# Performance work log

Measured on AMD Instinct MI355X. Metric: run time of the kernel, lower is better.

Reference implementation:

```python
import jax, jax.numpy as jnp
import numpy as np

B, N, K = 8, 4096, 16          # batch, points, kNN neighbors
IN_F, D, L, NUM_CLS = 3, 128, 2, 40  # in_features, hidden dim, transformer blocks, classes


def setup_inputs() -> dict:
    key = jax.random.key(0)
    ks = jax.random.split(key, 13)

    def w(k, shape):
        fan_in = shape[-2]
        return (jax.random.normal(k, shape, jnp.float32) / np.sqrt(fan_in).astype(np.float32))

    return {
        "features": jax.random.normal(ks[0], (B, N, IN_F), jnp.float32),
        "pos": jax.random.normal(ks[1], (B, N, 3), jnp.float32),
        "W_embed": w(ks[2], (IN_F, D)),
        "Wq": w(ks[3], (L, D, D)),
        "Wk": w(ks[4], (L, D, D)),
        "Wv": w(ks[5], (L, D, D)),
        "P1": w(ks[6], (L, 3, D)),   # position-encoding MLP layer 1
        "P2": w(ks[7], (L, D, D)),   # position-encoding MLP layer 2
        "G1": w(ks[8], (L, D, D)),   # attention (gamma) MLP layer 1
        "G2": w(ks[9], (L, D, D)),   # attention (gamma) MLP layer 2
        "Wo": w(ks[10], (L, D, D)),  # output projection per block
        "W_cls1": w(ks[11], (D, D)),
        "W_cls2": w(ks[12], (D, NUM_CLS)),
    }


def _gather(x, idx):
    # x: [B,N,C], idx: [B,N,K] -> [B,N,K,C]
    return jax.vmap(lambda xb, ib: xb[ib])(x, idx)


def _forward(features, pos, W_embed, Wq, Wk, Wv, P1, P2, G1, G2, Wo, W_cls1, W_cls2):
    # point-wise embedding MLP
    x = jax.nn.relu(features @ W_embed)  # [B,N,D]

    # kNN in euclidean space (indices, incl. self)
    sq = jnp.sum(pos * pos, axis=-1)                      # [B,N]
    d2 = sq[:, :, None] + sq[:, None, :] - 2.0 * jnp.einsum("bnc,bmc->bnm", pos, pos)
    _, idx = jax.lax.top_k(-d2, K)                        # [B,N,K]

    rel = pos[:, :, None, :] - _gather(pos, idx)          # [B,N,K,3]

    for l in range(L):
        q = x @ Wq[l]                                     # [B,N,D]
        k = x @ Wk[l]
        v = x @ Wv[l]
        kj = _gather(k, idx)                              # [B,N,K,D]
        vj = _gather(v, idx)
        # relative position encoding MLP
        delta = jax.nn.relu(rel @ P1[l]) @ P2[l]          # [B,N,K,D]
        # vector attention: gamma MLP over (q_i - k_j + delta)
        g = q[:, :, None, :] - kj + delta
        logits = jax.nn.relu(g @ G1[l]) @ G2[l]           # [B,N,K,D]
        attn = jax.nn.softmax(logits, axis=2)             # over K neighbors
        agg = jnp.sum(attn * (vj + delta), axis=2)        # [B,N,D]
        x = x + agg @ Wo[l]                               # residual

    pooled = jnp.max(x, axis=1)                           # [B,D] global max pool
    h = jax.nn.relu(pooled @ W_cls1)
    return h @ W_cls2                                     # [B,NUM_CLS]


def reference(features, pos, W_embed, Wq, Wk, Wv, P1, P2, G1, G2, Wo, W_cls1, W_cls2):
    return _forward(features, pos, W_embed, Wq, Wk, Wv, P1, P2, G1, G2, Wo, W_cls1, W_cls2)
```

## Files before the change

kernel.cpp:

```cpp
#include <hip/hip_runtime.h>
#include <float.h>

#define BB 8
#define NN 4096
#define KNN 16
#define Dh 128
#define NPTS (BB*NN)
#define NPART 8
#define PARTSZ (NN/NPART)

typedef __attribute__((ext_vector_type(8))) short bf16x8;
typedef __attribute__((ext_vector_type(8))) unsigned short u16x8;
typedef __attribute__((ext_vector_type(4))) float f32x4;

#define MFMA16(a,b,c) __builtin_amdgcn_mfma_f32_16x16x32_bf16(a,b,c,0,0,0)

__device__ __forceinline__ unsigned short f2b(float f) {
  union { float f; unsigned u; } v; v.f = f;
  unsigned r = v.u + 0x7fff + ((v.u >> 16) & 1);
  return (unsigned short)(r >> 16);
}
__device__ __forceinline__ float b2f(unsigned short s) {
  union { unsigned u; float f; } v; v.u = ((unsigned)s) << 16; return v.f;
}

__global__ __launch_bounds__(256) void embed_kernel(
    const float* __restrict__ f, const float* __restrict__ We, float* __restrict__ x) {
  int i = blockIdx.x * 256 + threadIdx.x;
  if (i >= NPTS * Dh) return;
  int p = i >> 7, d = i & 127;
  float f0 = f[p*3+0], f1 = f[p*3+1], f2 = f[p*3+2];
  float v = f0 * We[0*Dh + d] + f1 * We[1*Dh + d] + f2 * We[2*Dh + d];
  x[i] = fmaxf(v, 0.f);
}

__global__ __launch_bounds__(256) void knn_part_kernel(
    const float* __restrict__ pos, unsigned short* __restrict__ pidx) {
  __shared__ float4 cand[PARTSZ];
  int b = blockIdx.z, part = blockIdx.y;
  const float* pb = pos + (size_t)b * NN * 3;
  int c0 = part * PARTSZ;
  for (int i = threadIdx.x; i < PARTSZ; i += 256) {
    float X = pb[(c0+i)*3+0], Y = pb[(c0+i)*3+1], Z = pb[(c0+i)*3+2];
    cand[i] = make_float4(X, Y, Z, X*X + Y*Y + Z*Z);
  }
  __syncthreads();

  int q = blockIdx.x * 256 + threadIdx.x;
  float qx = pb[q*3+0], qy = pb[q*3+1], qz = pb[q*3+2];
  float qs = qx*qx + qy*qy + qz*qz;

  float val[KNN]; int ind[KNN];
  float cmax; int cslot;

  #pragma unroll
  for (int t = 0; t < KNN; t++) {
    float4 c = cand[t];
    val[t] = qs + c.w - 2.f*(qx*c.x + qy*c.y + qz*c.z);
    ind[t] = t;
  }
  cmax = val[0]; cslot = 0;
  #pragma unroll
  for (int i = 1; i < KNN; i++)
    if (val[i] >= cmax) { cmax = val[i]; cslot = i; }

  float bv0 = 0.f, bv1 = 0.f, bv2 = 0.f, bv3 = 0.f;
  int   bi0 = 0,   bi1 = 0,   bi2 = 0,   bi3 = 0;
  int   cnt = 0;

#define DRAIN_SLOT(S, BV, BI)                                      \
  { bool act = ((S) < cnt) && ((BV) < cmax);                       \
    if (__ballot(act)) {                                           \
      _Pragma("unroll")                                            \
      for (int i = 0; i < KNN; i++) {                              \
        bool r = act && (i == cslot);                              \
        val[i] = r ? (BV) : val[i];                                \
        ind[i] = r ? (BI) : ind[i];                                \
      }                                                            \
      cmax = val[0]; cslot = 0;                                    \
      _Pragma("unroll")                                            \
      for (int i = 1; i < KNN; i++)                                \
        if (val[i] >= cmax) { cmax = val[i]; cslot = i; }          \
    } }
#define DRAIN_ALL                                                  \
  { DRAIN_SLOT(0, bv0, bi0) DRAIN_SLOT(1, bv1, bi1)                \
    DRAIN_SLOT(2, bv2, bi2) DRAIN_SLOT(3, bv3, bi3) cnt = 0; }

  for (int m = KNN; m < PARTSZ; m++) {
    float4 c = cand[m];
    float d2 = qs + c.w - 2.f*(qx*c.x + qy*c.y + qz*c.z);
    if (d2 < cmax) {
      bv0 = (cnt == 0) ? d2 : bv0;  bi0 = (cnt == 0) ? m : bi0;
      bv1 = (cnt == 1) ? d2 : bv1;  bi1 = (cnt == 1) ? m : bi1;
      bv2 = (cnt == 2) ? d2 : bv2;  bi2 = (cnt == 2) ? m : bi2;
      bv3 = (cnt == 3) ? d2 : bv3;  bi3 = (cnt == 3) ? m : bi3;
      cnt++;
    }
    if (__ballot(cnt == 4)) DRAIN_ALL
  }
  if (__ballot(cnt > 0)) DRAIN_ALL

#undef DRAIN_SLOT
#undef DRAIN_ALL

  size_t base = ((size_t)(b*NN + q) * NPART + part) * KNN;
  #pragma unroll
  for (int i = 0; i < KNN; i++) pidx[base + i] = (unsigned short)(b*NN + c0 + ind[i]);
}

__global__ __launch_bounds__(256) void knn_merge_kernel(
    const float* __restrict__ pos, const unsigned short* __restrict__ pidx,
    unsigned short* __restrict__ idxout) {
  int p = blockIdx.x * 256 + threadIdx.x;
  float qx = pos[p*3+0], qy = pos[p*3+1], qz = pos[p*3+2];
  float qs = qx*qx + qy*qy + qz*qz;

  float val[KNN]; int ind[KNN];
  #pragma unroll
  for (int i = 0; i < KNN; i++) { val[i] = FLT_MAX; ind[i] = 0; }
  float cmax = FLT_MAX; int cslot = 0;

  for (int t = 0; t < NPART*KNN; t++) {
    int j = pidx[(size_t)p*NPART*KNN + t];
    float X = pos[j*3+0], Y = pos[j*3+1], Z = pos[j*3+2];
    float sq = X*X + Y*Y + Z*Z;
    float d2 = qs + sq - 2.f*(qx*X + qy*Y + qz*Z);
    if (d2 < cmax) {
      #pragma unroll
      for (int i = 0; i < KNN; i++) if (i == cslot) { val[i] = d2; ind[i] = j; }
      cmax = val[0]; cslot = 0;
      #pragma unroll
      for (int i = 1; i < KNN; i++) if (val[i] >= cmax) { cmax = val[i]; cslot = i; }
    }
  }
  #pragma unroll
  for (int i = 0; i < KNN; i++) idxout[(size_t)p*KNN + i] = (unsigned short)ind[i];
}

__global__ __launch_bounds__(256) void wprep_all_kernel(
    const float* __restrict__ W0, const float* __restrict__ W1,
    const float* __restrict__ W2, const float* __restrict__ W3,
    const float* __restrict__ W4, const float* __restrict__ W5,
    const float* __restrict__ W6, unsigned short* __restrict__ wT) {
  const float* srcs[7] = {W0, W1, W2, W3, W4, W5, W6};
  int z = blockIdx.z, m = blockIdx.y;
  const float* W = srcs[z] + m*16384;
  unsigned short* WT = wT + z*32768 + m*16384;
  int t = blockIdx.x * 256 + threadIdx.x;
  int o = t >> 7, i = t & 127;
  WT[o*128 + i] = f2b(W[i*128 + o]);
}

__global__ __launch_bounds__(256) void qkv_kernel(
    const float* __restrict__ x,
    const unsigned short* __restrict__ QT, const unsigned short* __restrict__ KT,
    const unsigned short* __restrict__ VT,
    unsigned short* __restrict__ qb, unsigned short* __restrict__ kb,
    unsigned short* __restrict__ vb) {
  int w = threadIdx.x >> 6, l = threadIdx.x & 63;
  int lr = l & 15, lg = l >> 4;
  int R = blockIdx.x * 64 + w * 16;
  const float* xr = x + (size_t)(R + lr) * Dh + lg * 8;
  bf16x8 a[4];
  #pragma unroll
  for (int kt = 0; kt < 4; kt++) {
    bf16x8 av;
    #pragma unroll
    for (int j = 0; j < 8; j++) av[j] = (short)f2b(xr[kt*32 + j]);
    a[kt] = av;
  }
  const unsigned short* Ws[3] = {QT, KT, VT};
  unsigned short* Os[3] = {qb, kb, vb};
  #pragma unroll
  for (int m = 0; m < 3; m++) {
    const unsigned short* W = Ws[m];
    unsigned short* O = Os[m];
    #pragma unroll
    for (int n = 0; n < 8; n++) {
      f32x4 c = {0.f, 0.f, 0.f, 0.f};
      #pragma unroll
      for (int kt = 0; kt < 4; kt++)
        c = MFMA16(a[kt], *(const bf16x8*)&W[(n*16 + lr)*Dh + kt*32 + lg*8], c);
      #pragma unroll
      for (int r = 0; r < 4; r++)
        O[(size_t)(R + lg*4 + r)*Dh + n*16 + lr] = f2b(c[r]);
    }
  }
}

__global__ __launch_bounds__(512, 2) void fused_mega_kernel(
    const unsigned short* __restrict__ qb, const unsigned short* __restrict__ kb,
    const unsigned short* __restrict__ vb,
    const unsigned short* __restrict__ idxb, const float* __restrict__ pos,
    const float* __restrict__ P1,
    const unsigned short* __restrict__ P2T, const unsigned short* __restrict__ G1T,
    const unsigned short* __restrict__ G2T, unsigned short* __restrict__ aggb) {
  __shared__ __align__(16) unsigned short wB[3][16384];
  __shared__ __align__(16) unsigned short trans[8][2048];
  int tid = threadIdx.x;
  int wv = tid >> 6, l = tid & 63;
  int lr = l & 15, lg = l >> 4;
  const int swz = (lr & 7) << 3;

  {
    const unsigned short* srcs[3] = {P2T, G1T, G2T};
    #pragma unroll
    for (int z = 0; z < 3; z++) {
      const unsigned short* src = srcs[z];
      for (int t = tid * 8; t < 16384; t += 512 * 8) {
        int dst = t ^ (((t >> 7) & 7) << 3);
        *(u16x8*)&wB[z][dst] = *(const u16x8*)&src[t];
      }
    }
  }
  __syncthreads();

  unsigned short* tb = trans[wv];
  int p0 = blockIdx.x * 128 + wv * 16;

  #pragma unroll 1
  for (int i = 0; i < 16; i++) {
    int p = p0 + i;

    int jA = idxb[(size_t)p*KNN + lr];
    int jC[4];
    #pragma unroll
    for (int r = 0; r < 4; r++) jC[r] = idxb[(size_t)p*KNN + lg*4 + r];

    float px0 = pos[p*3+0], py0 = pos[p*3+1], pz0 = pos[p*3+2];
    float rx = px0 - pos[jA*3+0], ry = py0 - pos[jA*3+1], rz = pz0 - pos[jA*3+2];

    bf16x8 aT[4];
    #pragma unroll
    for (int kt = 0; kt < 4; kt++) {
      bf16x8 av;
      #pragma unroll
      for (int j = 0; j < 8; j++) {
        int c = kt*32 + lg*8 + j;
        av[j] = (short)f2b(fmaxf(rx*P1[c] + ry*P1[Dh+c] + rz*P1[2*Dh+c], 0.f));
      }
      aT[kt] = av;
    }

    f32x4 dlt[8];
    #pragma unroll
    for (int n = 0; n < 8; n++) {
      f32x4 c = {0.f, 0.f, 0.f, 0.f};
      #pragma unroll
      for (int kt = 0; kt < 4; kt++)
        c = MFMA16(aT[kt], *(const bf16x8*)&wB[0][((n*16 + lr)*Dh + kt*32 + lg*8) ^ swz], c);
      dlt[n] = c;
    }

    #pragma unroll
    for (int n = 0; n < 8; n++) {
      float q = b2f(qb[(size_t)p*Dh + n*16 + lr]);
      #pragma unroll
      for (int r = 0; r < 4; r++) {
        float kj = b2f(kb[(size_t)jC[r]*Dh + n*16 + lr]);
        int row = lg*4 + r, ch = n*16 + lr;
        tb[(row*Dh + ch) ^ ((row & 7) << 3)] = f2b(q - kj + dlt[n][r]);
      }
    }

    bf16x8 ag[4];
    #pragma unroll
    for (int kt = 0; kt < 4; kt++)
      ag[kt] = *(const bf16x8*)&tb[(lr*Dh + kt*32 + lg*8) ^ swz];
    f32x4 hh[8];
    #pragma unroll
    for (int n = 0; n < 8; n++) {
      f32x4 c = {0.f, 0.f, 0.f, 0.f};
      #pragma unroll
      for (int kt = 0; kt < 4; kt++)
        c = MFMA16(ag[kt], *(const bf16x8*)&wB[1][((n*16 + lr)*Dh + kt*32 + lg*8) ^ swz], c);
      hh[n] = c;
    }
    #pragma unroll
    for (int n = 0; n < 8; n++) {
      #pragma unroll
      for (int r = 0; r < 4; r++) {
        int row = lg*4 + r, ch = n*16 + lr;
        tb[(row*Dh + ch) ^ ((row & 7) << 3)] = f2b(fmaxf(hh[n][r], 0.f));
      }
    }

    bf16x8 ah[4];
    #pragma unroll
    for (int kt = 0; kt < 4; kt++)
      ah[kt] = *(const bf16x8*)&tb[(lr*Dh + kt*32 + lg*8) ^ swz];
    f32x4 lgt[8];
    #pragma unroll
    for (int n = 0; n < 8; n++) {
      f32x4 c = {0.f, 0.f, 0.f, 0.f};
      #pragma unroll
      for (int kt = 0; kt < 4; kt++)
        c = MFMA16(ah[kt], *(const bf16x8*)&wB[2][((n*16 + lr)*Dh + kt*32 + lg*8) ^ swz], c);
      lgt[n] = c;
    }

    #pragma unroll
    for (int n = 0; n < 8; n++) {
      f32x4 L = lgt[n];
      float m = fmaxf(fmaxf(L[0], L[1]), fmaxf(L[2], L[3]));
      m = fmaxf(m, __shfl_xor(m, 16));
      m = fmaxf(m, __shfl_xor(m, 32));
      float e0 = __expf(L[0]-m), e1 = __expf(L[1]-m);
      float e2 = __expf(L[2]-m), e3 = __expf(L[3]-m);
      float s = e0 + e1 + e2 + e3;
      s += __shfl_xor(s, 16);
      s += __shfl_xor(s, 32);
      float inv = 1.f / s;
      float ws;
      ws  = e0 * (b2f(vb[(size_t)jC[0]*Dh + n*16 + lr]) + dlt[n][0]);
      ws += e1 * (b2f(vb[(size_t)jC[1]*Dh + n*16 + lr]) + dlt[n][1]);
      ws += e2 * (b2f(vb[(size_t)jC[2]*Dh + n*16 + lr]) + dlt[n][2]);
      ws += e3 * (b2f(vb[(size_t)jC[3]*Dh + n*16 + lr]) + dlt[n][3]);
      ws *= inv;
      ws += __shfl_xor(ws, 16);
      ws += __shfl_xor(ws, 32);
      if (lg == 0) aggb[(size_t)p*Dh + n*16 + lr] = f2b(ws);
    }
  }
}

__global__ __launch_bounds__(256) void xupd_kernel(
    float* __restrict__ x, const unsigned short* __restrict__ aggb,
    const unsigned short* __restrict__ WoT) {
  int w = threadIdx.x >> 6, l = threadIdx.x & 63;
  int lr = l & 15, lg = l >> 4;
  int R = blockIdx.x * 64 + w * 16;
  bf16x8 a[4];
  #pragma unroll
  for (int kt = 0; kt < 4; kt++)
    a[kt] = *(const bf16x8*)&aggb[(size_t)(R + lr)*Dh + kt*32 + lg*8];
  #pragma unroll
  for (int n = 0; n < 8; n++) {
    f32x4 c = {0.f, 0.f, 0.f, 0.f};
    #pragma unroll
    for (int kt = 0; kt < 4; kt++)
      c = MFMA16(a[kt], *(const bf16x8*)&WoT[(n*16 + lr)*Dh + kt*32 + lg*8], c);
    #pragma unroll
    for (int r = 0; r < 4; r++)
      x[(size_t)(R + lg*4 + r)*Dh + n*16 + lr] += c[r];
  }
}

__global__ __launch_bounds__(128) void pool_part_kernel(
    const float* __restrict__ x, float* __restrict__ part) {
  int b = blockIdx.y, chunk = blockIdx.x, d = threadIdx.x;
  const float* xb = x + ((size_t)b*NN + chunk*128) * Dh;
  float m = -FLT_MAX;
  for (int n = 0; n < 128; n++) m = fmaxf(m, xb[(size_t)n*Dh + d]);
  part[(b*32 + chunk)*Dh + d] = m;
}

__global__ __launch_bounds__(128) void head_kernel(
    const float* __restrict__ part, const float* __restrict__ W1,
    const float* __restrict__ W2, float* __restrict__ out) {
  int b = blockIdx.x, d = threadIdx.x;
  __shared__ float pooled[Dh], h[Dh];
  float m = -FLT_MAX;
  for (int c = 0; c < 32; c++) m = fmaxf(m, part[(b*32 + c)*Dh + d]);
  pooled[d] = m;
  __syncthreads();
  float acc = 0.f;
  for (int c = 0; c < Dh; c++) acc += pooled[c] * W1[c*Dh + d];
  h[d] = fmaxf(acc, 0.f);
  __syncthreads();
  if (d < 40) {
    float o = 0.f;
    for (int c = 0; c < Dh; c++) o += h[c] * W2[c*40 + d];
    out[b*40 + d] = o;
  }
}

extern "C" void kernel_launch(void* const* d_in, const int* in_sizes, int n_in,
                              void* d_out, int out_size, void* d_ws, size_t ws_size,
                              hipStream_t stream) {
  const float* features = (const float*)d_in[0];
  const float* pos      = (const float*)d_in[1];
  const float* W_embed  = (const float*)d_in[2];
  const float* Wq       = (const float*)d_in[3];
  const float* Wk       = (const float*)d_in[4];
  const float* Wv       = (const float*)d_in[5];
  const float* P1       = (const float*)d_in[6];
  const float* P2       = (const float*)d_in[7];
  const float* G1       = (const float*)d_in[8];
  const float* G2       = (const float*)d_in[9];
  const float* Wo       = (const float*)d_in[10];
  const float* Wc1      = (const float*)d_in[11];
  const float* Wc2      = (const float*)d_in[12];
  float* out = (float*)d_out;

  float* x = (float*)d_ws;
  unsigned short* qb = (unsigned short*)(x + (size_t)NPTS*Dh);
  unsigned short* kb = qb + (size_t)NPTS*Dh;
  unsigned short* vb = kb + (size_t)NPTS*Dh;
  unsigned short* wT = vb + (size_t)NPTS*Dh;
  unsigned short* aggb = wT + 7*2*16384;
  unsigned short* idxb = aggb + (size_t)NPTS*Dh;

  unsigned short* pidx = qb;
  float* part = (float*)qb;

  unsigned short* QT  = wT + 0*32768;
  unsigned short* KT  = wT + 1*32768;
  unsigned short* VT  = wT + 2*32768;
  unsigned short* P2T = wT + 3*32768;
  unsigned short* G1T = wT + 4*32768;
  unsigned short* G2T = wT + 5*32768;
  unsigned short* WoT = wT + 6*32768;

  knn_part_kernel<<<dim3(NN/256, NPART, BB), 256, 0, stream>>>(pos, pidx);
  knn_merge_kernel<<<NPTS/256, 256, 0, stream>>>(pos, pidx, idxb);

  wprep_all_kernel<<<dim3(64, 2, 7), 256, 0, stream>>>(Wq, Wk, Wv, P2, G1, G2, Wo, wT);
  embed_kernel<<<NPTS*Dh/256, 256, 0, stream>>>(features, W_embed, x);

  for (int l = 0; l < 2; l++) {
    qkv_kernel<<<NPTS/64, 256, 0, stream>>>(
        x, QT + l*16384, KT + l*16384, VT + l*16384, qb, kb, vb);
    fused_mega_kernel<<<256, 512, 0, stream>>>(
        qb, kb, vb, idxb, pos,
        P1 + l*3*Dh, P2T + l*16384, G1T + l*16384, G2T + l*16384, aggb);
    xupd_kernel<<<NPTS/64, 256, 0, stream>>>(x, aggb, WoT + l*16384);
  }

  pool_part_kernel<<<dim3(32, BB), 128, 0, stream>>>(x, part);
  head_kernel<<<BB, 128, 0, stream>>>(part, Wc1, Wc2, out);
}
```

Before: 995.1 us.

## Interleave K/V into packed buffer and prefetch next point's context in fused kernel

K and V projections are now stored interleaved as packed bf16 pairs, so one 32-bit gather per neighbour fetches both. The fused attention kernel loads all neighbour K/V values up front and prefetches the next point's indices, relative position and q values during the current iteration to hide gather latency. It also vectorises the P1 loads, changes the LDS swizzle pattern and switches to the HIP bf16 conversion intrinsic. The cost is higher register pressure from the prefetched context and the held kvr array, which under the 512-thread, 2-block launch bound could cause spills.

```diff
diff --git a/kernel.cpp b/kernel.cpp
--- a/kernel.cpp
+++ b/kernel.cpp
@@ -1,4 +1,5 @@
 #include <hip/hip_runtime.h>
+#include <hip/hip_bf16.h>
 #include <float.h>
 
 #define BB 8
@@ -16,13 +17,23 @@
 #define MFMA16(a,b,c) __builtin_amdgcn_mfma_f32_16x16x32_bf16(a,b,c,0,0,0)
 
 __device__ __forceinline__ unsigned short f2b(float f) {
-  union { float f; unsigned u; } v; v.f = f;
-  unsigned r = v.u + 0x7fff + ((v.u >> 16) & 1);
-  return (unsigned short)(r >> 16);
+  __hip_bfloat16 h = __float2bfloat16(f);
+  return *(unsigned short*)&h;
+}
+__device__ __forceinline__ unsigned pack_bf2(float lo, float hi) {
+  __hip_bfloat16 l = __float2bfloat16(lo), h = __float2bfloat16(hi);
+  return (unsigned)(*(unsigned short*)&l) | ((unsigned)(*(unsigned short*)&h) << 16);
 }
 __device__ __forceinline__ float b2f(unsigned short s) {
   union { unsigned u; float f; } v; v.u = ((unsigned)s) << 16; return v.f;
 }
+__device__ __forceinline__ float blo(unsigned u) {
+  union { unsigned u; float f; } v; v.u = u << 16; return v.f;
+}
+__device__ __forceinline__ float bhi(unsigned u) {
+  union { unsigned u; float f; } v; v.u = u & 0xffff0000u; return v.f;
+}
+__device__ __forceinline__ int swz16(int row) { return (row >> 2) << 4; }
 
 __global__ __launch_bounds__(256) void embed_kernel(
     const float* __restrict__ f, const float* __restrict__ We, float* __restrict__ x) {
@@ -155,8 +166,7 @@
     const float* __restrict__ x,
     const unsigned short* __restrict__ QT, const unsigned short* __restrict__ KT,
     const unsigned short* __restrict__ VT,
-    unsigned short* __restrict__ qb, unsigned short* __restrict__ kb,
-    unsigned short* __restrict__ vb) {
+    unsigned short* __restrict__ qb, unsigned* __restrict__ kvb) {
   int w = threadIdx.x >> 6, l = threadIdx.x & 63;
   int lr = l & 15, lg = l >> 4;
   int R = blockIdx.x * 64 + w * 16;
@@ -169,28 +179,51 @@
     for (int j = 0; j < 8; j++) av[j] = (short)f2b(xr[kt*32 + j]);
     a[kt] = av;
   }
-  const unsigned short* Ws[3] = {QT, KT, VT};
-  unsigned short* Os[3] = {qb, kb, vb};
-  #pragma unroll
-  for (int m = 0; m < 3; m++) {
-    const unsigned short* W = Ws[m];
-    unsigned short* O = Os[m];
-    #pragma unroll
-    for (int n = 0; n < 8; n++) {
-      f32x4 c = {0.f, 0.f, 0.f, 0.f};
-      #pragma unroll
-      for (int kt = 0; kt < 4; kt++)
-        c = MFMA16(a[kt], *(const bf16x8*)&W[(n*16 + lr)*Dh + kt*32 + lg*8], c);
-      #pragma unroll
-      for (int r = 0; r < 4; r++)
-        O[(size_t)(R + lg*4 + r)*Dh + n*16 + lr] = f2b(c[r]);
-    }
-  }
+  #pragma unroll
+  for (int n = 0; n < 8; n++) {
+    f32x4 c = {0.f, 0.f, 0.f, 0.f};
+    #pragma unroll
+    for (int kt = 0; kt < 4; kt++)
+      c = MFMA16(a[kt], *(const bf16x8*)&QT[(n*16 + lr)*Dh + kt*32 + lg*8], c);
+    #pragma unroll
+    for (int r = 0; r < 4; r++)
+      qb[(size_t)(R + lg*4 + r)*Dh + n*16 + lr] = f2b(c[r]);
+  }
+  #pragma unroll
+  for (int n = 0; n < 8; n++) {
+    f32x4 ck = {0.f, 0.f, 0.f, 0.f}, cv = {0.f, 0.f, 0.f, 0.f};
+    #pragma unroll
+    for (int kt = 0; kt < 4; kt++) {
+      ck = MFMA16(a[kt], *(const bf16x8*)&KT[(n*16 + lr)*Dh + kt*32 + lg*8], ck);
+      cv = MFMA16(a[kt], *(const bf16x8*)&VT[(n*16 + lr)*Dh + kt*32 + lg*8], cv);
+    }
+    #pragma unroll
+    for (int r = 0; r < 4; r++)
+      kvb[(size_t)(R + lg*4 + r)*Dh + n*16 + lr] = pack_bf2(ck[r], cv[r]);
+  }
+}
+
+struct PtCtx {
+  int jA, jC[4];
+  float rx, ry, rz;
+  unsigned short qv[8];
+};
+__device__ __forceinline__ void load_ctx(PtCtx& c, int p,
+    const unsigned short* __restrict__ idxb, const float* __restrict__ pos,
+    const unsigned short* __restrict__ qb, int lr, int lg) {
+  c.jA = idxb[(size_t)p*KNN + lr];
+  #pragma unroll
+  for (int r = 0; r < 4; r++) c.jC[r] = idxb[(size_t)p*KNN + lg*4 + r];
+  float px0 = pos[p*3+0], py0 = pos[p*3+1], pz0 = pos[p*3+2];
+  c.rx = px0 - pos[c.jA*3+0];
+  c.ry = py0 - pos[c.jA*3+1];
+  c.rz = pz0 - pos[c.jA*3+2];
+  #pragma unroll
+  for (int n = 0; n < 8; n++) c.qv[n] = qb[(size_t)p*Dh + n*16 + lr];
 }
 
 __global__ __launch_bounds__(512, 2) void fused_mega_kernel(
-    const unsigned short* __restrict__ qb, const unsigned short* __restrict__ kb,
-    const unsigned short* __restrict__ vb,
+    const unsigned short* __restrict__ qb, const unsigned* __restrict__ kvb,
     const unsigned short* __restrict__ idxb, const float* __restrict__ pos,
     const float* __restrict__ P1,
     const unsigned short* __restrict__ P2T, const unsigned short* __restrict__ G1T,
@@ -201,6 +234,7 @@
   int wv = tid >> 6, l = tid & 63;
   int lr = l & 15, lg = l >> 4;
   const int swz = (lr & 7) << 3;
+  const int swtR = swz16(lr);
 
   {
     const unsigned short* srcs[3] = {P2T, G1T, G2T};
@@ -218,27 +252,45 @@
   unsigned short* tb = trans[wv];
   int p0 = blockIdx.x * 128 + wv * 16;
 
+  PtCtx cur, nxt;
+  load_ctx(cur, p0, idxb, pos, qb, lr, lg);
+  nxt = cur;
+
   #pragma unroll 1
   for (int i = 0; i < 16; i++) {
     int p = p0 + i;
 
-    int jA = idxb[(size_t)p*KNN + lr];
-    int jC[4];
-    #pragma unroll
-    for (int r = 0; r < 4; r++) jC[r] = idxb[(size_t)p*KNN + lg*4 + r];
-
-    float px0 = pos[p*3+0], py0 = pos[p*3+1], pz0 = pos[p*3+2];
-    float rx = px0 - pos[jA*3+0], ry = py0 - pos[jA*3+1], rz = pz0 - pos[jA*3+2];
+    const unsigned* kvp0 = kvb + (size_t)cur.jC[0]*Dh;
+    const unsigned* kvp1 = kvb + (size_t)cur.jC[1]*Dh;
+    const unsigned* kvp2 = kvb + (size_t)cur.jC[2]*Dh;
+    const unsigned* kvp3 = kvb + (size_t)cur.jC[3]*Dh;
+    unsigned kvr[8][4];
+    #pragma unroll
+    for (int n = 0; n < 8; n++) {
+      kvr[n][0] = kvp0[n*16 + lr];
+      kvr[n][1] = kvp1[n*16 + lr];
+      kvr[n][2] = kvp2[n*16 + lr];
+      kvr[n][3] = kvp3[n*16 + lr];
+    }
+
+    if (i < 15) load_ctx(nxt, p + 1, idxb, pos, qb, lr, lg);
 
     bf16x8 aT[4];
     #pragma unroll
     for (int kt = 0; kt < 4; kt++) {
+      int c0 = kt*32 + lg*8;
+      float4 pa0 = *(const float4*)&P1[c0],        pa1 = *(const float4*)&P1[c0+4];
+      float4 pb0 = *(const float4*)&P1[Dh+c0],     pb1 = *(const float4*)&P1[Dh+c0+4];
+      float4 pc0 = *(const float4*)&P1[2*Dh+c0],   pc1 = *(const float4*)&P1[2*Dh+c0+4];
       bf16x8 av;
-      #pragma unroll
-      for (int j = 0; j < 8; j++) {
-        int c = kt*32 + lg*8 + j;
-        av[j] = (short)f2b(fmaxf(rx*P1[c] + ry*P1[Dh+c] + rz*P1[2*Dh+c], 0.f));
-      }
+      av[0] = (short)f2b(fmaxf(cur.rx*pa0.x + cur.ry*pb0.x + cur.rz*pc0.x, 0.f));
+      av[1] = (short)f2b(fmaxf(cur.rx*pa0.y + cur.ry*pb0.y + cur.rz*pc0.y, 0.f));
+      av[2] = (short)f2b(fmaxf(cur.rx*pa0.z + cur.ry*pb0.z + cur.rz*pc0.z, 0.f));
+      av[3] = (short)f2b(fmaxf(cur.rx*pa0.w + cur.ry*pb0.w + cur.rz*pc0.w, 0.f));
+      av[4] = (short)f2b(fmaxf(cur.rx*pa1.x + cur.ry*pb1.x + cur.rz*pc1.x, 0.f));
+      av[5] = (short)f2b(fmaxf(cur.rx*pa1.y + cur.ry*pb1.y + cur.rz*pc1.y, 0.f));
+      av[6] = (short)f2b(fmaxf(cur.rx*pa1.z + cur.ry*pb1.z + cur.rz*pc1.z, 0.f));
+      av[7] = (short)f2b(fmaxf(cur.rx*pa1.w + cur.ry*pb1.w + cur.rz*pc1.w, 0.f));
       aT[kt] = av;
     }
 
@@ -254,19 +306,18 @@
 
     #pragma unroll
     for (int n = 0; n < 8; n++) {
-      float q = b2f(qb[(size_t)p*Dh + n*16 + lr]);
+      float q = b2f(cur.qv[n]);
       #pragma unroll
       for (int r = 0; r < 4; r++) {
-        float kj = b2f(kb[(size_t)jC[r]*Dh + n*16 + lr]);
         int row = lg*4 + r, ch = n*16 + lr;
-        tb[(row*Dh + ch) ^ ((row & 7) << 3)] = f2b(q - kj + dlt[n][r]);
+        tb[(row*Dh + ch) ^ swz16(row)] = f2b(q - blo(kvr[n][r]) + dlt[n][r]);
       }
     }
 
     bf16x8 ag[4];
     #pragma unroll
     for (int kt = 0; kt < 4; kt++)
-      ag[kt] = *(const bf16x8*)&tb[(lr*Dh + kt*32 + lg*8) ^ swz];
+      ag[kt] = *(const bf16x8*)&tb[(lr*Dh + kt*32 + lg*8) ^ swtR];
     f32x4 hh[8];
     #pragma unroll
     for (int n = 0; n < 8; n++) {
@@ -281,14 +332,14 @@
       #pragma unroll
       for (int r = 0; r < 4; r++) {
         int row = lg*4 + r, ch = n*16 + lr;
-        tb[(row*Dh + ch) ^ ((row & 7) << 3)] = f2b(fmaxf(hh[n][r], 0.f));
+        tb[(row*Dh + ch) ^ swz16(row)] = f2b(fmaxf(hh[n][r], 0.f));
       }
     }
 
     bf16x8 ah[4];
     #pragma unroll
     for (int kt = 0; kt < 4; kt++)
-      ah[kt] = *(const bf16x8*)&tb[(lr*Dh + kt*32 + lg*8) ^ swz];
+      ah[kt] = *(const bf16x8*)&tb[(lr*Dh + kt*32 + lg*8) ^ swtR];
     f32x4 lgt[8];
     #pragma unroll
     for (int n = 0; n < 8; n++) {
@@ -312,15 +363,17 @@
       s += __shfl_xor(s, 32);
       float inv = 1.f / s;
       float ws;
-      ws  = e0 * (b2f(vb[(size_t)jC[0]*Dh + n*16 + lr]) + dlt[n][0]);
-      ws += e1 * (b2f(vb[(size_t)jC[1]*Dh + n*16 + lr]) + dlt[n][1]);
-      ws += e2 * (b2f(vb[(size_t)jC[2]*Dh + n*16 + lr]) + dlt[n][2]);
-      ws += e3 * (b2f(vb[(size_t)jC[3]*Dh + n*16 + lr]) + dlt[n][3]);
+      ws  = e0 * (bhi(kvr[n][0]) + dlt[n][0]);
+      ws += e1 * (bhi(kvr[n][1]) + dlt[n][1]);
+      ws += e2 * (bhi(kvr[n][2]) + dlt[n][2]);
+      ws += e3 * (bhi(kvr[n][3]) + dlt[n][3]);
       ws *= inv;
       ws += __shfl_xor(ws, 16);
       ws += __shfl_xor(ws, 32);
       if (lg == 0) aggb[(size_t)p*Dh + n*16 + lr] = f2b(ws);
     }
+
+    cur = nxt;
   }
 }
 
@@ -395,13 +448,12 @@
 
   float* x = (float*)d_ws;
   unsigned short* qb = (unsigned short*)(x + (size_t)NPTS*Dh);
-  unsigned short* kb = qb + (size_t)NPTS*Dh;
-  unsigned short* vb = kb + (size_t)NPTS*Dh;
-  unsigned short* wT = vb + (size_t)NPTS*Dh;
+  unsigned* kvb = (unsigned*)(qb + (size_t)NPTS*Dh);
+  unsigned short* wT = (unsigned short*)(kvb + (size_t)NPTS*Dh);
   unsigned short* aggb = wT + 7*2*16384;
   unsigned short* idxb = aggb + (size_t)NPTS*Dh;
 
-  unsigned short* pidx = qb;
+  unsigned short* pidx = (unsigned short*)kvb;
   float* part = (float*)qb;
 
   unsigned short* QT  = wT + 0*32768;
@@ -420,9 +472,9 @@
 
   for (int l = 0; l < 2; l++) {
     qkv_kernel<<<NPTS/64, 256, 0, stream>>>(
-        x, QT + l*16384, KT + l*16384, VT + l*16384, qb, kb, vb);
+        x, QT + l*16384, KT + l*16384, VT + l*16384, qb, kvb);
     fused_mega_kernel<<<256, 512, 0, stream>>>(
-        qb, kb, vb, idxb, pos,
+        qb, kvb, idxb, pos,
         P1 + l*3*Dh, P2T + l*16384, G1T + l*16384, G2T + l*16384, aggb);
     xupd_kernel<<<NPTS/64, 256, 0, stream>>>(x, aggb, WoT + l*16384);
   }
```

Result: faster. 944.6 us (-5.1%).
